# Performance work log

Measured on AMD Instinct MI355X. Metric: run time of the kernel, lower is better.

The kernel has to match this reference:

```python
import jax, jax.numpy as jnp
import numpy as np

D = 128          # embed_d
T = 10           # MAX_NEIGHBORS
L = 2            # n_layers
B = 4096
ND, FD = 20000, 2048
NG, FG = 20000, 1024
NC, FC = 10000, 512


def setup_inputs() -> dict:
    key = jax.random.key(0)
    ks = jax.random.split(key, 18)
    inp = {
        'drug_feats': jax.random.normal(ks[0], (ND, FD), jnp.float32),
        'gene_feats': jax.random.normal(ks[1], (NG, FG), jnp.float32),
        'cell_feats': jax.random.normal(ks[2], (NC, FC), jnp.float32),
        'Wd': jax.random.normal(ks[3], (FD, D), jnp.float32) / np.sqrt(FD),
        'bd': jnp.zeros((D,), jnp.float32),
        'Wg': jax.random.normal(ks[4], (FG, D), jnp.float32) / np.sqrt(FG),
        'bg': jnp.zeros((D,), jnp.float32),
        'Wc': jax.random.normal(ks[5], (FC, D), jnp.float32) / np.sqrt(FC),
        'bc': jnp.zeros((D,), jnp.float32),
        'gru_W': jax.random.normal(ks[6], (L, 3, D, 3 * D), jnp.float32) / np.sqrt(D),
        'gru_U': jax.random.normal(ks[7], (L, 3, D, 3 * D), jnp.float32) / np.sqrt(D),
        'gru_b': jnp.zeros((L, 3, 3 * D), jnp.float32),
        'att': jax.random.normal(ks[8], (L, 2 * D), jnp.float32) / np.sqrt(2 * D),
        'ids': jax.random.randint(ks[9], (B,), 0, ND, jnp.int32),
        # neighbor ids in [-1, N-1]; -1 == PAD_VALUE
        'neigh_drug': jax.random.randint(ks[10], (B, T), 0, ND + 1, jnp.int32) - 1,
        'neigh_gene': jax.random.randint(ks[11], (B, T), 0, NG + 1, jnp.int32) - 1,
        'neigh_cell': jax.random.randint(ks[12], (B, T), 0, NC + 1, jnp.int32) - 1,
    }
    return inp


def _proj_gather(table, W, b, idx):
    # gather raw features by id (PAD -> zeros) then project, matching
    # conteng_agg + masked scatter in node_het_agg.
    mask = (idx >= 0)                              # [B, T]
    safe = jnp.clip(idx, 0, None)
    f = table[safe] @ W + b                        # [B, T, D]
    return f * mask[..., None].astype(f.dtype), mask


def _gru_seq(x, W, U, b):
    # x: [B, T, D]; torch-style GRU, returns all hidden states [B, T, D]
    xw = jnp.einsum('btd,de->bte', x, W) + b       # [B, T, 3D]
    h0 = jnp.zeros((x.shape[0], U.shape[0]), x.dtype)

    def step(h, xt):
        hu = h @ U
        xz, xr, xn = jnp.split(xt, 3, axis=-1)
        hz, hr, hn = jnp.split(hu, 3, axis=-1)
        z = jax.nn.sigmoid(xz + hz)
        r = jax.nn.sigmoid(xr + hr)
        n = jnp.tanh(xn + r * hn)
        h = (1.0 - z) * n + z * h
        return h, h

    _, hs = jax.lax.scan(step, h0, jnp.swapaxes(xw, 0, 1))
    return jnp.swapaxes(hs, 0, 1)


def reference(drug_feats, gene_feats, cell_feats, Wd, bd, Wg, bg, Wc, bc,
              gru_W, gru_U, gru_b, att, ids, neigh_drug, neigh_gene, neigh_cell):
    # self embeddings: conteng_agg(batch_ids, drug_type)
    h = drug_feats[ids] @ Wd + bd                  # [B, D]

    # neighbor content features are the layer-0 projections every layer
    # (the torch code recomputes conteng_agg per layer; result is identical)
    neigh = [
        _proj_gather(drug_feats, Wd, bd, neigh_drug),
        _proj_gather(gene_feats, Wg, bg, neigh_gene),
        _proj_gather(cell_feats, Wc, bc, neigh_cell),
    ]

    for l in range(L):
        cands = [h]
        for t, (nf, mask) in enumerate(neigh):
            out = _gru_seq(nf, gru_W[l, t], gru_U[l, t], gru_b[l, t])  # [B,T,D]
            m = mask.astype(out.dtype)
            cnt = jnp.maximum(m.sum(-1, keepdims=True), 1.0)
            cands.append((out * m[..., None]).sum(1) / cnt)            # [B,D]
        C = jnp.stack(cands, axis=1)                                   # [B,4,D]
        cat = jnp.concatenate(
            [jnp.broadcast_to(h[:, None, :], C.shape), C], axis=-1)    # [B,4,2D]
        w = jax.nn.softmax(jax.nn.leaky_relu(cat @ att[l]), axis=-1)   # [B,4]
        h = jnp.einsum('bk,bkd->bd', w, C)
    return h
```

## Files before the change

kernel.cpp:

```cpp
#include <hip/hip_runtime.h>
#include <stdint.h>


typedef short bf16x8 __attribute__((ext_vector_type(8)));
typedef float f32x4  __attribute__((ext_vector_type(4)));

__device__ __forceinline__ short f2bf(float f) {
  union { float f; unsigned u; } v; v.f = f;
  unsigned r = (v.u + 0x7fffu + ((v.u >> 16) & 1u)) >> 16;
  return (short)r;
}
__device__ __forceinline__ float b2f(short s) {
  union { float f; unsigned u; } v; v.u = ((unsigned)(unsigned short)s) << 16;
  return v.f;
}
__device__ __forceinline__ f32x4 mfma_bf16(bf16x8 a, bf16x8 b, f32x4 c) {
  return __builtin_amdgcn_mfma_f32_16x16x32_bf16(a, b, c, 0, 0, 0);
}

__global__ __launch_bounds__(256) void prep_t(const float* __restrict__ src,
                                              short* __restrict__ dst,
                                              int K, int N) {
  const size_t slice = (size_t)K * N;
  const float* s = src + blockIdx.y * slice;
  short* d = dst + blockIdx.y * slice;
  int i = blockIdx.x * 256 + threadIdx.x;
  if (i < K * N) {
    int k = i / N, n = i - k * N;
    d[(size_t)n * K + k] = f2bf(s[i]);
  }
}

__global__ __launch_bounds__(256) void proj_kernel(
    const float* __restrict__ A, const short* __restrict__ Wt,
    const float* __restrict__ bias, short* __restrict__ Pb,
    float* __restrict__ Pf, int M, int K) {
  __shared__ alignas(16) short As[32][136];
  __shared__ alignas(16) short Bs[128][136];
  const int tid  = threadIdx.x;
  const int lane = tid & 63;
  const int w    = tid >> 6;
  const int wc   = w * 32;
  const int quad = lane >> 4;
  const int ln   = lane & 15;
  const int m0   = blockIdx.x * 32;

  const int arow = tid >> 3;
  const int akc  = (tid & 7) * 16;
  const int brow = tid >> 1;
  const int bkc  = (tid & 1) * 64;

  const int kIters = K >> 7;
  const int krot   = blockIdx.x % kIters;
  const int gr     = m0 + arow;
  const bool aok   = gr < M;
  const float* arp = A + (size_t)gr * K + akc;

  float4 areg[4];
  auto loadA = [&](int k0) {
    if (aok) {
      const float4* p = (const float4*)(arp + k0);
      areg[0] = p[0]; areg[1] = p[1]; areg[2] = p[2]; areg[3] = p[3];
    } else {
      float4 z = {0.f, 0.f, 0.f, 0.f};
      areg[0] = z; areg[1] = z; areg[2] = z; areg[3] = z;
    }
  };

  f32x4 acc[2][2];
#pragma unroll
  for (int i = 0; i < 2; i++)
#pragma unroll
    for (int j = 0; j < 2; j++) acc[i][j] = (f32x4){0.f, 0.f, 0.f, 0.f};

  loadA(krot << 7);

  for (int it = 0; it < kIters; it++) {
    int ks = krot + it; if (ks >= kIters) ks -= kIters;
    const int k0 = ks << 7;
    {
      bf16x8 v0, v1;
      v0[0]=f2bf(areg[0].x); v0[1]=f2bf(areg[0].y); v0[2]=f2bf(areg[0].z); v0[3]=f2bf(areg[0].w);
      v0[4]=f2bf(areg[1].x); v0[5]=f2bf(areg[1].y); v0[6]=f2bf(areg[1].z); v0[7]=f2bf(areg[1].w);
      v1[0]=f2bf(areg[2].x); v1[1]=f2bf(areg[2].y); v1[2]=f2bf(areg[2].z); v1[3]=f2bf(areg[2].w);
      v1[4]=f2bf(areg[3].x); v1[5]=f2bf(areg[3].y); v1[6]=f2bf(areg[3].z); v1[7]=f2bf(areg[3].w);
      *(bf16x8*)&As[arow][akc]     = v0;
      *(bf16x8*)&As[arow][akc + 8] = v1;
    }
    {
      const short* bp = Wt + (size_t)brow * K + k0 + bkc;
#pragma unroll
      for (int j = 0; j < 8; j++)
        *(bf16x8*)&Bs[brow][bkc + j * 8] = *(const bf16x8*)(bp + j * 8);
    }
    __syncthreads();
    if (it + 1 < kIters) {
      int kn = krot + it + 1; if (kn >= kIters) kn -= kIters;
      loadA(kn << 7);
    }
#pragma unroll
    for (int kt = 0; kt < 4; kt++) {
      bf16x8 af[2], bfr[2];
#pragma unroll
      for (int mi = 0; mi < 2; mi++)
        af[mi] = *(const bf16x8*)&As[mi * 16 + ln][kt * 32 + quad * 8];
#pragma unroll
      for (int nj = 0; nj < 2; nj++)
        bfr[nj] = *(const bf16x8*)&Bs[wc + nj * 16 + ln][kt * 32 + quad * 8];
#pragma unroll
      for (int mi = 0; mi < 2; mi++)
#pragma unroll
        for (int nj = 0; nj < 2; nj++)
          acc[mi][nj] = mfma_bf16(af[mi], bfr[nj], acc[mi][nj]);
    }
    __syncthreads();
  }

#pragma unroll
  for (int mi = 0; mi < 2; mi++)
#pragma unroll
    for (int nj = 0; nj < 2; nj++) {
      const int col = wc + nj * 16 + ln;
      const float bv = bias[col];
#pragma unroll
      for (int r = 0; r < 4; r++) {
        const int row = m0 + mi * 16 + quad * 4 + r;
        if (row < M) {
          const float v = acc[mi][nj][r] + bv;
          if (Pb) Pb[(size_t)row * 128 + col] = f2bf(v);
          if (Pf) Pf[(size_t)row * 128 + col] = v;
        }
      }
    }
}

__global__ __launch_bounds__(256) void gather_h0(const float* __restrict__ Pd,
                                                 const int* __restrict__ ids,
                                                 float* __restrict__ h) {
  int i = blockIdx.x * 256 + threadIdx.x;
  int b = i >> 7, d = i & 127;
  h[i] = Pd[(size_t)ids[b] * 128 + d];
}

__global__ __launch_bounds__(256) void xw_kernel(
    const short* __restrict__ Pb, const float* __restrict__ Pf,
    const int* __restrict__ nbr, const short* __restrict__ Wts,
    const float* __restrict__ gbs, short* __restrict__ xwT) {
  __shared__ alignas(16) short As[64][136];
  __shared__ alignas(16) short Bs[128][136];
  const int tid  = threadIdx.x;
  const int lane = tid & 63;
  const int w    = tid >> 6;
  const int wr   = (w >> 1) * 32;
  const int wc   = (w & 1) * 64;
  const int quad = lane >> 4;
  const int ln   = lane & 15;
  const int m0    = blockIdx.x * 64;
  const int nbase = blockIdx.y * 128;

  {
    const int row = tid >> 2;
    const int kc  = (tid & 3) * 32;
    const int idx = nbr[m0 + row];
    if (idx >= 0) {
      if (Pb) {
        const short* p = Pb + (size_t)idx * 128 + kc;
#pragma unroll
        for (int i = 0; i < 4; i++)
          *(bf16x8*)&As[row][kc + i * 8] = *(const bf16x8*)(p + i * 8);
      } else {
        const float* p = Pf + (size_t)idx * 128 + kc;
#pragma unroll
        for (int i = 0; i < 4; i++) {
          float4 v0 = *(const float4*)(p + i * 8);
          float4 v1 = *(const float4*)(p + i * 8 + 4);
          bf16x8 bv;
          bv[0]=f2bf(v0.x); bv[1]=f2bf(v0.y); bv[2]=f2bf(v0.z); bv[3]=f2bf(v0.w);
          bv[4]=f2bf(v1.x); bv[5]=f2bf(v1.y); bv[6]=f2bf(v1.z); bv[7]=f2bf(v1.w);
          *(bf16x8*)&As[row][kc + i * 8] = bv;
        }
      }
    } else {
      bf16x8 zv;
#pragma unroll
      for (int i = 0; i < 8; i++) zv[i] = 0;
#pragma unroll
      for (int i = 0; i < 4; i++) *(bf16x8*)&As[row][kc + i * 8] = zv;
    }
  }
  {
    const int n  = tid >> 1;
    const int kc = (tid & 1) * 64;
    const short* p = Wts + (size_t)(nbase + n) * 128 + kc;
#pragma unroll
    for (int i = 0; i < 8; i++)
      *(bf16x8*)&Bs[n][kc + i * 8] = *(const bf16x8*)(p + i * 8);
  }
  __syncthreads();

  f32x4 acc[2][4];
#pragma unroll
  for (int i = 0; i < 2; i++)
#pragma unroll
    for (int j = 0; j < 4; j++) acc[i][j] = (f32x4){0.f, 0.f, 0.f, 0.f};

#pragma unroll
  for (int kt = 0; kt < 4; kt++) {
    bf16x8 af[2], bfr[4];
#pragma unroll
    for (int mi = 0; mi < 2; mi++)
      af[mi] = *(const bf16x8*)&As[wr + mi * 16 + ln][kt * 32 + quad * 8];
#pragma unroll
    for (int nj = 0; nj < 4; nj++)
      bfr[nj] = *(const bf16x8*)&Bs[wc + nj * 16 + ln][kt * 32 + quad * 8];
#pragma unroll
    for (int mi = 0; mi < 2; mi++)
#pragma unroll
      for (int nj = 0; nj < 4; nj++)
        acc[mi][nj] = mfma_bf16(af[mi], bfr[nj], acc[mi][nj]);
  }

#pragma unroll
  for (int mi = 0; mi < 2; mi++)
#pragma unroll
    for (int nj = 0; nj < 4; nj++) {
      const int col = wc + nj * 16 + ln;
      const float bv = gbs[nbase + col];
#pragma unroll
      for (int r = 0; r < 4; r++) {
        const int rt   = m0 + wr + mi * 16 + quad * 4 + r;
        const int grow = rt / 10;
        const int st   = rt - grow * 10;
        xwT[((size_t)st * 4096 + grow) * 384 + nbase + col] =
            f2bf(acc[mi][nj][r] + bv);
      }
    }
}

__global__ __launch_bounds__(256) void scan_kernel(
    const short* __restrict__ xwT, const short* __restrict__ Utz,
    const int* __restrict__ nbr, float* __restrict__ outp) {
  __shared__ alignas(16) short hs[16][128];
  __shared__ alignas(16) short xls[16][392];
  __shared__ float mask_s[16][10];
  __shared__ float cinv[16];

  const int tid  = threadIdx.x;
  const int lane = tid & 63;
  const int w    = tid >> 6;
  const int nb   = w * 32;
  const int quad = lane >> 4;
  const int ln   = lane & 15;
  const int r0   = blockIdx.x * 16;

  if (tid < 160) {
    int i = tid / 10, t = tid % 10;
    mask_s[i][t] = (nbr[(r0 + i) * 10 + t] >= 0) ? 1.f : 0.f;
  }
  {
    short* hf = &hs[0][0];
    for (int i = tid; i < 16 * 128; i += 256) hf[i] = 0;
  }
  __syncthreads();
  if (tid < 16) {
    float s = 0.f;
    for (int t = 0; t < 10; t++) s += mask_s[tid][t];
    cinv[tid] = 1.f / fmaxf(s, 1.f);
  }

  bf16x8 u[3][2][4];
#pragma unroll
  for (int g = 0; g < 3; g++)
#pragma unroll
    for (int jj = 0; jj < 2; jj++)
#pragma unroll
      for (int kt = 0; kt < 4; kt++)
        u[g][jj][kt] = *(const bf16x8*)(Utz +
            (size_t)(g * 128 + nb + jj * 16 + ln) * 128 + kt * 32 + quad * 8);

  int srow[3], scol[3];
#pragma unroll
  for (int j = 0; j < 3; j++) {
    const int o = tid * 24 + j * 8;
    srow[j] = o / 384;
    scol[j] = o - srow[j] * 384;
  }

  float hreg[2][4], oacc[2][4];
#pragma unroll
  for (int jj = 0; jj < 2; jj++)
#pragma unroll
    for (int r = 0; r < 4; r++) { hreg[jj][r] = 0.f; oacc[jj][r] = 0.f; }

  __syncthreads();

  for (int st = 0; st < 10; st++) {
    bf16x8 a[4];
#pragma unroll
    for (int kt = 0; kt < 4; kt++)
      a[kt] = *(const bf16x8*)&hs[ln][kt * 32 + quad * 8];

    const short* src = xwT + ((size_t)st * 4096 + r0) * 384;
    bf16x8 xrg[3];
#pragma unroll
    for (int j = 0; j < 3; j++)
      xrg[j] = *(const bf16x8*)(src + tid * 24 + j * 8);

    f32x4 hu[3][2];
#pragma unroll
    for (int g = 0; g < 3; g++)
#pragma unroll
      for (int jj = 0; jj < 2; jj++) hu[g][jj] = (f32x4){0.f, 0.f, 0.f, 0.f};
#pragma unroll
    for (int kt = 0; kt < 4; kt++)
#pragma unroll
      for (int g = 0; g < 3; g++)
#pragma unroll
        for (int jj = 0; jj < 2; jj++)
          hu[g][jj] = mfma_bf16(a[kt], u[g][jj][kt], hu[g][jj]);

#pragma unroll
    for (int j = 0; j < 3; j++)
      *(bf16x8*)&xls[srow[j]][scol[j]] = xrg[j];
    __syncthreads();

#pragma unroll
    for (int jj = 0; jj < 2; jj++) {
      const int col = nb + jj * 16 + ln;
#pragma unroll
      for (int r = 0; r < 4; r++) {
        const int row = quad * 4 + r;
        const float xz = b2f(xls[row][col]);
        const float xr = b2f(xls[row][col + 128]);
        const float xn = b2f(xls[row][col + 256]);
        const float zg = 1.f / (1.f + __expf(-(xz + hu[0][jj][r])));
        const float rg = 1.f / (1.f + __expf(-(xr + hu[1][jj][r])));
        const float pn = xn + rg * hu[2][jj][r];
        const float e2 = __expf(2.f * pn);
        const float n  = (e2 - 1.f) / (e2 + 1.f);
        const float hn = (1.f - zg) * n + zg * hreg[jj][r];
        hreg[jj][r] = hn;
        oacc[jj][r] += hn * mask_s[row][st];
        hs[row][col] = f2bf(hn);
      }
    }
    __syncthreads();
  }

#pragma unroll
  for (int jj = 0; jj < 2; jj++)
#pragma unroll
    for (int r = 0; r < 4; r++) {
      const int row = quad * 4 + r;
      outp[(size_t)(r0 + row) * 128 + nb + jj * 16 + ln] =
          oacc[jj][r] * cinv[row];
    }
}

__global__ __launch_bounds__(256) void attn_kernel(
    const float* __restrict__ hin, const float* __restrict__ cand,
    const float* __restrict__ att, float* __restrict__ hout) {
  const int tid  = threadIdx.x;
  const int lane = tid & 63;
  const int w    = tid >> 6;
  const int gb   = blockIdx.x * 4 + w;

  const float ah0 = att[lane],       ah1 = att[lane + 64];
  const float ac0 = att[128 + lane], ac1 = att[192 + lane];

  float c0[4], c1[4];
  c0[0] = hin[(size_t)gb * 128 + lane];
  c1[0] = hin[(size_t)gb * 128 + 64 + lane];
#pragma unroll
  for (int k = 1; k < 4; k++) {
    const float* p = cand + (size_t)(k - 1) * 4096 * 128 + (size_t)gb * 128;
    c0[k] = p[lane]; c1[k] = p[64 + lane];
  }

  float sh = ah0 * c0[0] + ah1 * c1[0];
#pragma unroll
  for (int m = 1; m < 64; m <<= 1) sh += __shfl_xor(sh, m);

  float e[4];
#pragma unroll
  for (int k = 0; k < 4; k++) {
    float s = ac0 * c0[k] + ac1 * c1[k];
#pragma unroll
    for (int m = 1; m < 64; m <<= 1) s += __shfl_xor(s, m);
    s += sh;
    e[k] = (s > 0.f) ? s : 0.01f * s;
  }
  const float mx = fmaxf(fmaxf(e[0], e[1]), fmaxf(e[2], e[3]));
  float wk[4], wsum = 0.f;
#pragma unroll
  for (int k = 0; k < 4; k++) { wk[k] = __expf(e[k] - mx); wsum += wk[k]; }
  const float inv = 1.f / wsum;
  float o0 = 0.f, o1 = 0.f;
#pragma unroll
  for (int k = 0; k < 4; k++) { o0 += wk[k] * c0[k]; o1 += wk[k] * c1[k]; }
  hout[(size_t)gb * 128 + lane]      = o0 * inv;
  hout[(size_t)gb * 128 + 64 + lane] = o1 * inv;
}

extern "C" void kernel_launch(void* const* d_in, const int* in_sizes, int n_in,
                              void* d_out, int out_size, void* d_ws, size_t ws_size,
                              hipStream_t stream) {
  const float* drug = (const float*)d_in[0];
  const float* gene = (const float*)d_in[1];
  const float* cell = (const float*)d_in[2];
  const float* Wd   = (const float*)d_in[3];
  const float* bd   = (const float*)d_in[4];
  const float* Wg   = (const float*)d_in[5];
  const float* bg   = (const float*)d_in[6];
  const float* Wc   = (const float*)d_in[7];
  const float* bc   = (const float*)d_in[8];
  const float* gruW = (const float*)d_in[9];
  const float* gruU = (const float*)d_in[10];
  const float* grub = (const float*)d_in[11];
  const float* att  = (const float*)d_in[12];
  const int* ids    = (const int*)d_in[13];
  const int* nbr[3] = {(const int*)d_in[14], (const int*)d_in[15],
                       (const int*)d_in[16]};

  char* ws = (char*)d_ws;
  auto alloc = [&](size_t bytes) {
    void* p = ws; ws += (bytes + 255) & ~(size_t)255; return p;
  };
  float* Pdf  = (float*)alloc((size_t)20000 * 128 * 4);
  short* Pgb  = (short*)alloc((size_t)20000 * 128 * 2);
  short* Pcb  = (short*)alloc((size_t)10000 * 128 * 2);
  float* h    = (float*)alloc((size_t)4096 * 128 * 4);
  float* cand = (float*)alloc((size_t)3 * 4096 * 128 * 4);
  short* xwb  = (short*)alloc((size_t)40960 * 384 * 2);
  short* Wdt  = (short*)alloc((size_t)2048 * 128 * 2);
  short* Wgt  = (short*)alloc((size_t)1024 * 128 * 2);
  short* Wct  = (short*)alloc((size_t)512 * 128 * 2);
  short* gWt  = (short*)alloc((size_t)6 * 384 * 128 * 2);
  short* Ut   = (short*)alloc((size_t)6 * 384 * 128 * 2);

  prep_t<<<dim3(1024, 1), 256, 0, stream>>>(Wd, Wdt, 2048, 128);
  prep_t<<<dim3(512, 1),  256, 0, stream>>>(Wg, Wgt, 1024, 128);
  prep_t<<<dim3(256, 1),  256, 0, stream>>>(Wc, Wct, 512, 128);
  prep_t<<<dim3(192, 6),  256, 0, stream>>>(gruW, gWt, 128, 384);
  prep_t<<<dim3(192, 6),  256, 0, stream>>>(gruU, Ut,  128, 384);

  proj_kernel<<<625, 256, 0, stream>>>(drug, Wdt, bd, nullptr, Pdf, 20000, 2048);
  proj_kernel<<<625, 256, 0, stream>>>(gene, Wgt, bg, Pgb, nullptr, 20000, 1024);
  proj_kernel<<<313, 256, 0, stream>>>(cell, Wct, bc, Pcb, nullptr, 10000, 512);
  gather_h0<<<2048, 256, 0, stream>>>(Pdf, ids, h);

  const short* Ptab_b[3] = {nullptr, Pgb, Pcb};
  const float* Ptab_f[3] = {Pdf, nullptr, nullptr};
  for (int l = 0; l < 2; l++) {
    for (int t = 0; t < 3; t++) {
      const int s = l * 3 + t;
      xw_kernel<<<dim3(640, 3), 256, 0, stream>>>(
          Ptab_b[t], Ptab_f[t], nbr[t], gWt + (size_t)s * 49152,
          grub + (size_t)s * 384, xwb);
      scan_kernel<<<256, 256, 0, stream>>>(
          xwb, Ut + (size_t)s * 49152, nbr[t], cand + (size_t)t * 4096 * 128);
    }
    attn_kernel<<<1024, 256, 0, stream>>>(
        h, cand, att + l * 256, (l == 1) ? (float*)d_out : h);
  }
}
```

Measured before the change: 672.9 us.

## Batch all GRU layers/types into single launches and merge prep/projection kernels

Merges the three weight-transpose launches and the two GRU-weight preps into two launches, and the three projection GEMMs into one grid-indexed launch. Because the GRU inputs never depend on h, all six xw GEMMs and all six scans run as one launch each when the workspace is large enough. The drug projection also gets a bf16 copy, so the gather path no longer converts fp32 on the fly. This removes launch serialization and lets small grids fill the GPU, at the cost of a much larger workspace for the six xw slots.

```diff
diff --git a/kernel.cpp b/kernel.cpp
--- a/kernel.cpp
+++ b/kernel.cpp
@@ -18,23 +18,49 @@
   return __builtin_amdgcn_mfma_f32_16x16x32_bf16(a, b, c, 0, 0, 0);
 }
 
-__global__ __launch_bounds__(256) void prep_t(const float* __restrict__ src,
-                                              short* __restrict__ dst,
-                                              int K, int N) {
-  const size_t slice = (size_t)K * N;
-  const float* s = src + blockIdx.y * slice;
-  short* d = dst + blockIdx.y * slice;
+struct PrepW { const float* src[3]; short* dst[3]; int K[3]; };
+
+__global__ __launch_bounds__(256) void prep_w(PrepW a) {
+  const int y = blockIdx.y;
+  const int K = a.K[y];
   int i = blockIdx.x * 256 + threadIdx.x;
-  if (i < K * N) {
-    int k = i / N, n = i - k * N;
-    d[(size_t)n * K + k] = f2bf(s[i]);
-  }
-}
-
-__global__ __launch_bounds__(256) void proj_kernel(
-    const float* __restrict__ A, const short* __restrict__ Wt,
-    const float* __restrict__ bias, short* __restrict__ Pb,
-    float* __restrict__ Pf, int M, int K) {
+  if (i < K * 128) {
+    int k = i >> 7, n = i & 127;
+    a.dst[y][(size_t)n * K + k] = f2bf(a.src[y][i]);
+  }
+}
+
+__global__ __launch_bounds__(256) void prep_gru(const float* __restrict__ W,
+                                                const float* __restrict__ U,
+                                                short* __restrict__ dW,
+                                                short* __restrict__ dU) {
+  const int y = blockIdx.y;
+  const float* s = (y < 6) ? W + (size_t)y * 49152 : U + (size_t)(y - 6) * 49152;
+  short* d       = (y < 6) ? dW + (size_t)y * 49152 : dU + (size_t)(y - 6) * 49152;
+  int i = blockIdx.x * 256 + threadIdx.x;
+  if (i < 49152) {
+    int k = i / 384, n = i - k * 384;
+    d[(size_t)n * 128 + k] = f2bf(s[i]);
+  }
+}
+
+struct ProjA {
+  const float* A[3]; const short* Wt[3]; const float* bias[3];
+  short* Pb[3]; float* Pf[3]; int M[3]; int K[3];
+};
+
+__global__ __launch_bounds__(256) void proj_all(ProjA p) {
+  const int y = blockIdx.y;
+  const int M = p.M[y];
+  const int m0 = blockIdx.x * 32;
+  if (m0 >= M) return;
+  const int K = p.K[y];
+  const float* A    = p.A[y];
+  const short* Wt   = p.Wt[y];
+  const float* bias = p.bias[y];
+  short* Pb         = p.Pb[y];
+  float* Pf         = p.Pf[y];
+
   __shared__ alignas(16) short As[32][136];
   __shared__ alignas(16) short Bs[128][136];
   const int tid  = threadIdx.x;
@@ -43,7 +69,6 @@
   const int wc   = w * 32;
   const int quad = lane >> 4;
   const int ln   = lane & 15;
-  const int m0   = blockIdx.x * 32;
 
   const int arow = tid >> 3;
   const int akc  = (tid & 7) * 16;
@@ -59,8 +84,8 @@
   float4 areg[4];
   auto loadA = [&](int k0) {
     if (aok) {
-      const float4* p = (const float4*)(arp + k0);
-      areg[0] = p[0]; areg[1] = p[1]; areg[2] = p[2]; areg[3] = p[3];
+      const float4* ptr = (const float4*)(arp + k0);
+      areg[0] = ptr[0]; areg[1] = ptr[1]; areg[2] = ptr[2]; areg[3] = ptr[3];
     } else {
       float4 z = {0.f, 0.f, 0.f, 0.f};
       areg[0] = z; areg[1] = z; areg[2] = z; areg[3] = z;
@@ -142,10 +167,20 @@
   h[i] = Pd[(size_t)ids[b] * 128 + d];
 }
 
-__global__ __launch_bounds__(256) void xw_kernel(
-    const short* __restrict__ Pb, const float* __restrict__ Pf,
-    const int* __restrict__ nbr, const short* __restrict__ Wts,
-    const float* __restrict__ gbs, short* __restrict__ xwT) {
+__global__ __launch_bounds__(256) void xw_all(
+    const short* __restrict__ P0, const short* __restrict__ P1,
+    const short* __restrict__ P2, const int* __restrict__ n0,
+    const int* __restrict__ n1, const int* __restrict__ n2,
+    const short* __restrict__ gWt_all, const float* __restrict__ grub_all,
+    short* __restrict__ xwT_base, int s_base) {
+  const int s  = s_base + blockIdx.z;
+  const int ty = s - (s / 3) * 3;
+  const short* Pb  = (ty == 0) ? P0 : (ty == 1) ? P1 : P2;
+  const int*   nbr = (ty == 0) ? n0 : (ty == 1) ? n1 : n2;
+  const short* Wts = gWt_all + (size_t)s * 49152;
+  const float* gbs = grub_all + (size_t)s * 384;
+  short* xwT = xwT_base + (size_t)blockIdx.z * 40960 * 384;
+
   __shared__ alignas(16) short As[64][136];
   __shared__ alignas(16) short Bs[128][136];
   const int tid  = threadIdx.x;
@@ -163,23 +198,10 @@
     const int kc  = (tid & 3) * 32;
     const int idx = nbr[m0 + row];
     if (idx >= 0) {
-      if (Pb) {
-        const short* p = Pb + (size_t)idx * 128 + kc;
-#pragma unroll
-        for (int i = 0; i < 4; i++)
-          *(bf16x8*)&As[row][kc + i * 8] = *(const bf16x8*)(p + i * 8);
-      } else {
-        const float* p = Pf + (size_t)idx * 128 + kc;
-#pragma unroll
-        for (int i = 0; i < 4; i++) {
-          float4 v0 = *(const float4*)(p + i * 8);
-          float4 v1 = *(const float4*)(p + i * 8 + 4);
-          bf16x8 bv;
-          bv[0]=f2bf(v0.x); bv[1]=f2bf(v0.y); bv[2]=f2bf(v0.z); bv[3]=f2bf(v0.w);
-          bv[4]=f2bf(v1.x); bv[5]=f2bf(v1.y); bv[6]=f2bf(v1.z); bv[7]=f2bf(v1.w);
-          *(bf16x8*)&As[row][kc + i * 8] = bv;
-        }
-      }
+      const short* p = Pb + (size_t)idx * 128 + kc;
+#pragma unroll
+      for (int i = 0; i < 4; i++)
+        *(bf16x8*)&As[row][kc + i * 8] = *(const bf16x8*)(p + i * 8);
     } else {
       bf16x8 zv;
 #pragma unroll
@@ -237,9 +259,18 @@
     }
 }
 
-__global__ __launch_bounds__(256) void scan_kernel(
-    const short* __restrict__ xwT, const short* __restrict__ Utz,
-    const int* __restrict__ nbr, float* __restrict__ outp) {
+__global__ __launch_bounds__(256) void scan_all(
+    const short* __restrict__ xwT_base, const short* __restrict__ Ut_base,
+    const int* __restrict__ n0, const int* __restrict__ n1,
+    const int* __restrict__ n2, float* __restrict__ out_base, int s_base) {
+  const int sz = blockIdx.y;
+  const int s  = s_base + sz;
+  const int ty = s - (s / 3) * 3;
+  const short* xwT = xwT_base + (size_t)sz * 40960 * 384;
+  const short* Utz = Ut_base + (size_t)s * 49152;
+  const int*   nbr = (ty == 0) ? n0 : (ty == 1) ? n1 : n2;
+  float* outp = out_base + (size_t)sz * 4096 * 128;
+
   __shared__ alignas(16) short hs[16][128];
   __shared__ alignas(16) short xls[16][392];
   __shared__ float mask_s[16][10];
@@ -254,8 +285,8 @@
   const int r0   = blockIdx.x * 16;
 
   if (tid < 160) {
-    int i = tid / 10, t = tid % 10;
-    mask_s[i][t] = (nbr[(r0 + i) * 10 + t] >= 0) ? 1.f : 0.f;
+    int i = tid / 10, tt = tid % 10;
+    mask_s[i][tt] = (nbr[(r0 + i) * 10 + tt] >= 0) ? 1.f : 0.f;
   }
   {
     short* hf = &hs[0][0];
@@ -263,9 +294,9 @@
   }
   __syncthreads();
   if (tid < 16) {
-    float s = 0.f;
-    for (int t = 0; t < 10; t++) s += mask_s[tid][t];
-    cinv[tid] = 1.f / fmaxf(s, 1.f);
+    float sm = 0.f;
+    for (int tt = 0; tt < 10; tt++) sm += mask_s[tid][tt];
+    cinv[tid] = 1.f / fmaxf(sm, 1.f);
   }
 
   bf16x8 u[3][2][4];
@@ -384,11 +415,11 @@
   float e[4];
 #pragma unroll
   for (int k = 0; k < 4; k++) {
-    float s = ac0 * c0[k] + ac1 * c1[k];
-#pragma unroll
-    for (int m = 1; m < 64; m <<= 1) s += __shfl_xor(s, m);
-    s += sh;
-    e[k] = (s > 0.f) ? s : 0.01f * s;
+    float sv = ac0 * c0[k] + ac1 * c1[k];
+#pragma unroll
+    for (int m = 1; m < 64; m <<= 1) sv += __shfl_xor(sv, m);
+    sv += sh;
+    e[k] = (sv > 0.f) ? sv : 0.01f * sv;
   }
   const float mx = fmaxf(fmaxf(e[0], e[1]), fmaxf(e[2], e[3]));
   float wk[4], wsum = 0.f;
@@ -422,45 +453,74 @@
   const int* nbr[3] = {(const int*)d_in[14], (const int*)d_in[15],
                        (const int*)d_in[16]};
 
+  const size_t XW_SLOT   = (size_t)40960 * 384;
+  const size_t CAND_SLOT = (size_t)4096 * 128;
+
+  const size_t need_big =
+      (size_t)20000 * 128 * 4 + (size_t)20000 * 128 * 2 +
+      (size_t)20000 * 128 * 2 + (size_t)10000 * 128 * 2 +
+      (size_t)4096 * 128 * 4 + 6 * CAND_SLOT * 4 + 6 * XW_SLOT * 2 +
+      (size_t)2048 * 128 * 2 + (size_t)1024 * 128 * 2 + (size_t)512 * 128 * 2 +
+      2 * (size_t)6 * 384 * 128 * 2 + 16384 ;
+  const bool big = ws_size >= need_big;
+
   char* ws = (char*)d_ws;
   auto alloc = [&](size_t bytes) {
     void* p = ws; ws += (bytes + 255) & ~(size_t)255; return p;
   };
   float* Pdf  = (float*)alloc((size_t)20000 * 128 * 4);
+  short* Pdb  = (short*)alloc((size_t)20000 * 128 * 2);
   short* Pgb  = (short*)alloc((size_t)20000 * 128 * 2);
   short* Pcb  = (short*)alloc((size_t)10000 * 128 * 2);
   float* h    = (float*)alloc((size_t)4096 * 128 * 4);
-  float* cand = (float*)alloc((size_t)3 * 4096 * 128 * 4);
-  short* xwb  = (short*)alloc((size_t)40960 * 384 * 2);
+  float* cand = (float*)alloc((big ? 6 : 3) * CAND_SLOT * 4);
+  short* xwb  = (short*)alloc((big ? 6 : 1) * XW_SLOT * 2);
   short* Wdt  = (short*)alloc((size_t)2048 * 128 * 2);
   short* Wgt  = (short*)alloc((size_t)1024 * 128 * 2);
   short* Wct  = (short*)alloc((size_t)512 * 128 * 2);
   short* gWt  = (short*)alloc((size_t)6 * 384 * 128 * 2);
   short* Ut   = (short*)alloc((size_t)6 * 384 * 128 * 2);
 
-  prep_t<<<dim3(1024, 1), 256, 0, stream>>>(Wd, Wdt, 2048, 128);
-  prep_t<<<dim3(512, 1),  256, 0, stream>>>(Wg, Wgt, 1024, 128);
-  prep_t<<<dim3(256, 1),  256, 0, stream>>>(Wc, Wct, 512, 128);
-  prep_t<<<dim3(192, 6),  256, 0, stream>>>(gruW, gWt, 128, 384);
-  prep_t<<<dim3(192, 6),  256, 0, stream>>>(gruU, Ut,  128, 384);
-
-  proj_kernel<<<625, 256, 0, stream>>>(drug, Wdt, bd, nullptr, Pdf, 20000, 2048);
-  proj_kernel<<<625, 256, 0, stream>>>(gene, Wgt, bg, Pgb, nullptr, 20000, 1024);
-  proj_kernel<<<313, 256, 0, stream>>>(cell, Wct, bc, Pcb, nullptr, 10000, 512);
+  {
+    PrepW pw;
+    pw.src[0] = Wd;  pw.dst[0] = Wdt; pw.K[0] = 2048;
+    pw.src[1] = Wg;  pw.dst[1] = Wgt; pw.K[1] = 1024;
+    pw.src[2] = Wc;  pw.dst[2] = Wct; pw.K[2] = 512;
+    prep_w<<<dim3(1024, 3), 256, 0, stream>>>(pw);
+  }
+  prep_gru<<<dim3(192, 12), 256, 0, stream>>>(gruW, gruU, gWt, Ut);
+
+  {
+    ProjA pa;
+    pa.A[0] = drug; pa.Wt[0] = Wdt; pa.bias[0] = bd;
+    pa.Pb[0] = Pdb; pa.Pf[0] = Pdf; pa.M[0] = 20000; pa.K[0] = 2048;
+    pa.A[1] = gene; pa.Wt[1] = Wgt; pa.bias[1] = bg;
+    pa.Pb[1] = Pgb; pa.Pf[1] = nullptr; pa.M[1] = 20000; pa.K[1] = 1024;
+    pa.A[2] = cell; pa.Wt[2] = Wct; pa.bias[2] = bc;
+    pa.Pb[2] = Pcb; pa.Pf[2] = nullptr; pa.M[2] = 10000; pa.K[2] = 512;
+    proj_all<<<dim3(625, 3), 256, 0, stream>>>(pa);
+  }
   gather_h0<<<2048, 256, 0, stream>>>(Pdf, ids, h);
 
-  const short* Ptab_b[3] = {nullptr, Pgb, Pcb};
-  const float* Ptab_f[3] = {Pdf, nullptr, nullptr};
-  for (int l = 0; l < 2; l++) {
-    for (int t = 0; t < 3; t++) {
-      const int s = l * 3 + t;
-      xw_kernel<<<dim3(640, 3), 256, 0, stream>>>(
-          Ptab_b[t], Ptab_f[t], nbr[t], gWt + (size_t)s * 49152,
-          grub + (size_t)s * 384, xwb);
-      scan_kernel<<<256, 256, 0, stream>>>(
-          xwb, Ut + (size_t)s * 49152, nbr[t], cand + (size_t)t * 4096 * 128);
-    }
+  if (big) {
+    xw_all<<<dim3(640, 3, 6), 256, 0, stream>>>(
+        Pdb, Pgb, Pcb, nbr[0], nbr[1], nbr[2], gWt, grub, xwb, 0);
+    scan_all<<<dim3(256, 6), 256, 0, stream>>>(
+        xwb, Ut, nbr[0], nbr[1], nbr[2], cand, 0);
+    attn_kernel<<<1024, 256, 0, stream>>>(h, cand, att, h);
     attn_kernel<<<1024, 256, 0, stream>>>(
-        h, cand, att + l * 256, (l == 1) ? (float*)d_out : h);
-  }
-}
+        h, cand + 3 * CAND_SLOT, att + 256, (float*)d_out);
+  } else {
+    for (int l = 0; l < 2; l++) {
+      for (int t = 0; t < 3; t++) {
+        const int s = l * 3 + t;
+        xw_all<<<dim3(640, 3, 1), 256, 0, stream>>>(
+            Pdb, Pgb, Pcb, nbr[0], nbr[1], nbr[2], gWt, grub, xwb, s);
+        scan_all<<<dim3(256, 1), 256, 0, stream>>>(
+            xwb, Ut, nbr[0], nbr[1], nbr[2], cand + (size_t)t * CAND_SLOT, s);
+      }
+      attn_kernel<<<1024, 256, 0, stream>>>(
+          h, cand, att + l * 256, (l == 1) ? (float*)d_out : h);
+    }
+  }
+}
```

After: 543.3 us. 19.3% less time.
